# Optimization experiments

Measured on AMD Instinct MI355X. Metric: run time of the kernel, lower is better.

## Reference

```python
import jax, jax.numpy as jnp
import numpy as np

N = 50000
D = 128
E = 625000
EPS = 1e-15
BALL_EPS = 1e-5


def _logmap0(x, c):
    # Poincare ball log map at origin: artanh(sqrt(c)||x||) * x / (sqrt(c)||x||)
    sqrt_c = jnp.sqrt(c)
    xn = jnp.clip(jnp.linalg.norm(x, axis=-1, keepdims=True), EPS)
    arg = jnp.clip(sqrt_c * xn, -1.0 + BALL_EPS, 1.0 - BALL_EPS)
    return jnp.arctanh(arg) * x / (sqrt_c * xn)


def _expmap0(u, c):
    # Poincare ball exp map at origin: tanh(sqrt(c)||u||) * u / (sqrt(c)||u||)
    sqrt_c = jnp.sqrt(c)
    un = jnp.clip(jnp.linalg.norm(u, axis=-1, keepdims=True), EPS)
    return jnp.tanh(sqrt_c * un) * u / (sqrt_c * un)


def setup_inputs() -> dict:
    key = jax.random.key(0)
    ks = jax.random.split(key, 10)
    scale = 0.01  # keep points well inside the Poincare ball
    node_embeddings = jax.random.normal(ks[0], (N, D), jnp.float32) * scale
    hist1 = jax.random.normal(ks[1], (N, D), jnp.float32) * scale
    hist2 = jax.random.normal(ks[2], (N, D), jnp.float32) * scale
    hist3 = jax.random.normal(ks[3], (N, D), jnp.float32) * scale
    lin_w = jax.random.normal(ks[4], (D, D), jnp.float32) * (1.0 / np.sqrt(D))
    lin_b = jnp.zeros((D,), jnp.float32)
    conv_w = jax.random.normal(ks[5], (D, D, 3), jnp.float32) * (1.0 / np.sqrt(3 * D))
    conv_b = jnp.zeros((D,), jnp.float32)
    curvature = jnp.array([-1.0], jnp.float32)
    edge_src = jax.random.randint(ks[6], (E,), 0, N, jnp.int32)
    edge_dst = jax.random.randint(ks[7], (E,), 0, N, jnp.int32)
    return {
        'node_embeddings': node_embeddings,
        'hist1': hist1, 'hist2': hist2, 'hist3': hist3,
        'lin_w': lin_w, 'lin_b': lin_b,
        'conv_w': conv_w, 'conv_b': conv_b,
        'curvature': curvature,
        'edge_src': edge_src, 'edge_dst': edge_dst,
    }


def reference(node_embeddings, hist1, hist2, hist3, lin_w, lin_b,
              conv_w, conv_b, curvature, edge_src, edge_dst):
    c = jnp.abs(curvature[0])

    # --- HyperbolicDiffusionGraphConv ---
    tangent = _logmap0(node_embeddings, c)                       # [N, D]
    transformed = tangent @ lin_w.T + lin_b                      # [N, D]
    msgs = transformed[edge_src]                                 # [E, D] gather
    summed = jax.ops.segment_sum(msgs, edge_dst, num_segments=N)  # [N, D] scatter
    deg = jax.ops.segment_sum(jnp.ones((E,), jnp.float32), edge_dst, num_segments=N)
    neigh = jnp.where(deg[:, None] > 0, summed / jnp.clip(deg[:, None], 1.0), 0.0)
    current_emb = _expmap0(neigh, c)                             # [N, D]

    # --- HyperbolicDilatedCausalConv (3-step history, kernel_size=3 -> length 1) ---
    tangent_cur = _logmap0(current_emb, c)
    th = jnp.stack([_logmap0(hist1, c), _logmap0(hist2, c), _logmap0(hist3, c)], axis=2)  # [N, D, 3]
    # Conv1d(D -> D, k=3) on length-3 input reduces to a single contraction.
    conv_out = jnp.einsum('nik,oik->no', th, conv_w) + conv_b    # [N, D]
    return _expmap0(conv_out + tangent_cur, c)
```

## Files before the change

kernel.cpp:

```cpp
#include <hip/hip_runtime.h>

#define N_NODES 50000
#define DIM 128
#define N_EDGES 625000
#define EBLK 2442
#define SLOTS 96
#define CSTRIDE 16

#define SC_BLOCKS 25000
#define PK_BLOCKS 256
#define ZR_BLOCKS 196
#define SETUP_BLOCKS (SC_BLOCKS + PK_BLOCKS + ZR_BLOCKS)

typedef float f32x4 __attribute__((ext_vector_type(4)));
typedef short s16x8 __attribute__((ext_vector_type(8)));

__device__ __forceinline__ unsigned short f2bf(float f) {
    unsigned u = __builtin_bit_cast(unsigned, f);
    unsigned r = (u + 0x7fffu + ((u >> 16) & 1u)) >> 16;
    return (unsigned short)r;
}
__device__ __forceinline__ float lo_bf(unsigned u) {
    return __builtin_bit_cast(float, u << 16);
}
__device__ __forceinline__ float hi_bf(unsigned u) {
    return __builtin_bit_cast(float, u & 0xffff0000u);
}

__device__ __forceinline__ void gload_lds16(const unsigned short* g, unsigned short* l) {
    __builtin_amdgcn_global_load_lds(
        (const __attribute__((address_space(1))) void*)g,
        (__attribute__((address_space(3))) void*)l, 16, 0, 0);
}

__device__ __forceinline__ float logmap_scale(float ss, float sc) {
    float xn = fmaxf(sqrtf(ss), 1e-15f);
    float arg = fminf(sc * xn, 1.0f - 1e-5f);
    if (arg < 0.25f) {
        float z2 = arg * arg;
        return 1.0f + z2 * (0.33333333f + z2 * (0.2f + z2 * 0.14285715f));
    }
    float at = 0.5f * log1pf(2.0f * arg / (1.0f - arg));
    return at / (sc * xn);
}

__global__ __launch_bounds__(256) void k_setup(
    const float* __restrict__ node, const float* __restrict__ h1,
    const float* __restrict__ h2, const float* __restrict__ h3,
    const float* __restrict__ lin_w, const float* __restrict__ conv_w,
    const float* __restrict__ curv,
    unsigned short* __restrict__ node_t, unsigned short* __restrict__ A,
    unsigned short* __restrict__ Wt, int* __restrict__ cnt) {
    int b = blockIdx.x;
    int tid = threadIdx.x;
    if (b < SC_BLOCKS) {
        int row = b * 8 + (tid >> 5);
        int g = tid & 31;
        int a = row / N_NODES;
        int n = row - a * N_NODES;
        const float* src = (a == 0) ? node : (a == 1) ? h1 : (a == 2) ? h2 : h3;
        float4 x = ((const float4*)&src[n * DIM])[g];
        float ss = x.x * x.x + x.y * x.y + x.z * x.z + x.w * x.w;
        ss += __shfl_xor(ss, 1, 64);
        ss += __shfl_xor(ss, 2, 64);
        ss += __shfl_xor(ss, 4, 64);
        ss += __shfl_xor(ss, 8, 64);
        ss += __shfl_xor(ss, 16, 64);
        float c = fabsf(curv[0]);
        float s = logmap_scale(ss, sqrtf(c));
        unsigned short o0 = f2bf(x.x * s), o1 = f2bf(x.y * s);
        unsigned short o2 = f2bf(x.z * s), o3 = f2bf(x.w * s);
        uint2 ov;
        ov.x = (unsigned)o0 | ((unsigned)o1 << 16);
        ov.y = (unsigned)o2 | ((unsigned)o3 << 16);
        if (a == 0) {
            *(uint2*)&node_t[n * DIM + g * 4] = ov;
        } else {
            *(uint2*)&A[n * 512 + a * 128 + g * 4] = ov;
        }
    } else if (b < SC_BLOCKS + PK_BLOCKS) {
        int idx = (b - SC_BLOCKS) * 256 + tid;
        int o = idx >> 9;
        int k = idx & 511;
        float v;
        if (k < 128) {
            v = lin_w[o * 128 + k];
        } else {
            int kk = (k - 128) >> 7;
            int i = (k - 128) & 127;
            v = conv_w[o * 384 + i * 3 + kk];
        }
        Wt[idx] = f2bf(v);
    } else {
        int i = (b - SC_BLOCKS - PK_BLOCKS) * 256 + tid;
        if (i < N_NODES) cnt[i * CSTRIDE] = 0;
    }
}

__global__ void k_bucket(const int* __restrict__ esrc, const int* __restrict__ edst,
                         int* __restrict__ cnt, unsigned short* __restrict__ slots) {
    int e = blockIdx.x * 256 + threadIdx.x;
    if (e >= N_EDGES) return;
    int d = edst[e];
    int pos = __hip_atomic_fetch_add(&cnt[d * CSTRIDE], 1, __ATOMIC_RELAXED,
                                     __HIP_MEMORY_SCOPE_AGENT);
    if (pos < SLOTS) slots[d * SLOTS + pos] = (unsigned short)esrc[e];
}

__global__ __launch_bounds__(256) void k_gather(
    const unsigned short* __restrict__ slots, const int* __restrict__ cnt,
    const unsigned short* __restrict__ node_t, unsigned short* __restrict__ A) {
    int n = blockIdx.x * 8 + (threadIdx.x >> 5);
    int lane = threadIdx.x & 31;
    int ctrue = cnt[n * CSTRIDE];
    int c = ctrue < SLOTS ? ctrue : SLOTS;
    const unsigned short* row = &slots[n * SLOTS];
    float p0 = 0.f, p1 = 0.f, p2 = 0.f, p3 = 0.f;
    float q0 = 0.f, q1 = 0.f, q2 = 0.f, q3 = 0.f;
    for (int base = 0; base < c; base += 32) {
        int rem = c - base;
        int m = rem < 32 ? rem : 32;
        int my = (int)row[base + (lane < m ? lane : m - 1)];
        for (int i = 0; i < m; i += 8) {
            int i1 = i + 1 < m ? i + 1 : m - 1;
            int i2 = i + 2 < m ? i + 2 : m - 1;
            int i3 = i + 3 < m ? i + 3 : m - 1;
            int i4 = i + 4 < m ? i + 4 : m - 1;
            int i5 = i + 5 < m ? i + 5 : m - 1;
            int i6 = i + 6 < m ? i + 6 : m - 1;
            int i7 = i + 7 < m ? i + 7 : m - 1;
            int s0 = __shfl(my, i, 32),  s1 = __shfl(my, i1, 32);
            int s2 = __shfl(my, i2, 32), s3 = __shfl(my, i3, 32);
            int s4 = __shfl(my, i4, 32), s5 = __shfl(my, i5, 32);
            int s6 = __shfl(my, i6, 32), s7 = __shfl(my, i7, 32);
            uint2 u0 = *(const uint2*)&node_t[s0 * DIM + lane * 4];
            uint2 u1 = *(const uint2*)&node_t[s1 * DIM + lane * 4];
            uint2 u2 = *(const uint2*)&node_t[s2 * DIM + lane * 4];
            uint2 u3 = *(const uint2*)&node_t[s3 * DIM + lane * 4];
            uint2 u4 = *(const uint2*)&node_t[s4 * DIM + lane * 4];
            uint2 u5 = *(const uint2*)&node_t[s5 * DIM + lane * 4];
            uint2 u6 = *(const uint2*)&node_t[s6 * DIM + lane * 4];
            uint2 u7 = *(const uint2*)&node_t[s7 * DIM + lane * 4];
            p0 += lo_bf(u0.x); p1 += hi_bf(u0.x); p2 += lo_bf(u0.y); p3 += hi_bf(u0.y);
            if (i + 1 < m) { q0 += lo_bf(u1.x); q1 += hi_bf(u1.x); q2 += lo_bf(u1.y); q3 += hi_bf(u1.y); }
            if (i + 2 < m) { p0 += lo_bf(u2.x); p1 += hi_bf(u2.x); p2 += lo_bf(u2.y); p3 += hi_bf(u2.y); }
            if (i + 3 < m) { q0 += lo_bf(u3.x); q1 += hi_bf(u3.x); q2 += lo_bf(u3.y); q3 += hi_bf(u3.y); }
            if (i + 4 < m) { p0 += lo_bf(u4.x); p1 += hi_bf(u4.x); p2 += lo_bf(u4.y); p3 += hi_bf(u4.y); }
            if (i + 5 < m) { q0 += lo_bf(u5.x); q1 += hi_bf(u5.x); q2 += lo_bf(u5.y); q3 += hi_bf(u5.y); }
            if (i + 6 < m) { p0 += lo_bf(u6.x); p1 += hi_bf(u6.x); p2 += lo_bf(u6.y); p3 += hi_bf(u6.y); }
            if (i + 7 < m) { q0 += lo_bf(u7.x); q1 += hi_bf(u7.x); q2 += lo_bf(u7.y); q3 += hi_bf(u7.y); }
        }
    }
    float t0 = p0 + q0, t1 = p1 + q1, t2 = p2 + q2, t3 = p3 + q3;
    float inv = (ctrue > 0) ? 1.0f / (float)ctrue : 0.0f;
    unsigned short o0 = f2bf(t0 * inv), o1 = f2bf(t1 * inv);
    unsigned short o2 = f2bf(t2 * inv), o3 = f2bf(t3 * inv);
    uint2 ov;
    ov.x = (unsigned)o0 | ((unsigned)o1 << 16);
    ov.y = (unsigned)o2 | ((unsigned)o3 << 16);
    *(uint2*)&A[n * 512 + lane * 4] = ov;
}

#define RB 128
#define BK 64
__global__ __launch_bounds__(256) void k_gemm(
    const unsigned short* __restrict__ A, const int* __restrict__ deg,
    const unsigned short* __restrict__ Wt,
    const float* __restrict__ lin_b, const float* __restrict__ conv_b,
    const float* __restrict__ curv, float* __restrict__ out) {
    __shared__ __align__(16) unsigned short As[2][RB * BK];
    __shared__ __align__(16) unsigned short Bs[2][128 * BK];
    int tid = threadIdx.x;
    int n0 = blockIdx.x * RB;
    int w = tid >> 6;
    int lane = tid & 63;
    int ml = lane & 15;
    int q = lane >> 4;
    int lr = lane >> 3;
    int lj = lane & 7;

    f32x4 acc[2][8];
    #pragma unroll
    for (int rt = 0; rt < 2; ++rt)
        #pragma unroll
        for (int i = 0; i < 8; ++i) acc[rt][i] = (f32x4){0.f, 0.f, 0.f, 0.f};

    #pragma unroll
    for (int t = 0; t < 4; ++t) {
        int m = t * 4 + w;
        int r = m * 8 + lr;
        int jg = lj ^ (r & 7);
        gload_lds16(A + (n0 + r) * 512 + jg * 8, &As[0][m * 512]);
    }
    #pragma unroll
    for (int t = 0; t < 4; ++t) {
        int m = t * 4 + w;
        int r = m * 8 + lr;
        int jg = lj ^ (r & 7);
        gload_lds16(Wt + r * 512 + jg * 8, &Bs[0][m * 512]);
    }

    #pragma unroll
    for (int kk = 0; kk < 8; ++kk) {
        int cur = kk & 1;
        __syncthreads();
        if (kk < 7) {
            int nb = cur ^ 1;
            #pragma unroll
            for (int t = 0; t < 4; ++t) {
                int m = t * 4 + w;
                int r = m * 8 + lr;
                int jg = lj ^ (r & 7);
                gload_lds16(A + (n0 + r) * 512 + (kk + 1) * 64 + jg * 8, &As[nb][m * 512]);
            }
            #pragma unroll
            for (int t = 0; t < 4; ++t) {
                int m = t * 4 + w;
                int r = m * 8 + lr;
                int jg = lj ^ (r & 7);
                gload_lds16(Wt + r * 512 + (kk + 1) * 64 + jg * 8, &Bs[nb][m * 512]);
            }
        }
        __builtin_amdgcn_s_setprio(1);
        #pragma unroll
        for (int ks = 0; ks < 2; ++ks) {
            int ca = ((ks * 4 + q) ^ (ml & 7)) * 8;
            s16x8 a0 = *(const s16x8*)&As[cur][(w * 32 + ml) * BK + ca];
            s16x8 a1 = *(const s16x8*)&As[cur][(w * 32 + 16 + ml) * BK + ca];
            #pragma unroll
            for (int ct = 0; ct < 8; ++ct) {
                s16x8 bb = *(const s16x8*)&Bs[cur][(ct * 16 + ml) * BK + ca];
                acc[0][ct] = __builtin_amdgcn_mfma_f32_16x16x32_bf16(a0, bb, acc[0][ct], 0, 0, 0);
                acc[1][ct] = __builtin_amdgcn_mfma_f32_16x16x32_bf16(a1, bb, acc[1][ct], 0, 0, 0);
            }
        }
        __builtin_amdgcn_s_setprio(0);
    }

    float c = fabsf(curv[0]);
    float sc = sqrtf(c);
    float cb[8], lb[8];
    #pragma unroll
    for (int ct = 0; ct < 8; ++ct) {
        cb[ct] = conv_b[ct * 16 + ml];
        lb[ct] = lin_b[ct * 16 + ml];
    }
    #pragma unroll
    for (int rt = 0; rt < 2; ++rt) {
        #pragma unroll
        for (int r = 0; r < 4; ++r) {
            int n = n0 + w * 32 + rt * 16 + q * 4 + r;
            bool valid = (n < N_NODES);
            float dgf = 0.f;
            if (valid) dgf = (deg[n * CSTRIDE] > 0) ? 1.0f : 0.0f;
            float y[8];
            float ssq = 0.f;
            #pragma unroll
            for (int ct = 0; ct < 8; ++ct) {
                float v = acc[rt][ct][r] + cb[ct] + dgf * lb[ct];
                y[ct] = v;
                ssq += v * v;
            }
            ssq += __shfl_xor(ssq, 1, 64);
            ssq += __shfl_xor(ssq, 2, 64);
            ssq += __shfl_xor(ssq, 4, 64);
            ssq += __shfl_xor(ssq, 8, 64);
            float un = fmaxf(sqrtf(ssq), 1e-15f);
            float z = sc * un;
            float os;
            if (z < 0.25f) {
                float z2 = z * z;
                os = 1.0f + z2 * (-0.33333333f + z2 * (0.13333333f - z2 * 0.053968254f));
            } else {
                os = tanhf(z) / z;
            }
            if (valid) {
                #pragma unroll
                for (int ct = 0; ct < 8; ++ct)
                    out[n * DIM + ct * 16 + ml] = y[ct] * os;
            }
        }
    }
}

extern "C" void kernel_launch(void* const* d_in, const int* in_sizes, int n_in,
                              void* d_out, int out_size, void* d_ws, size_t ws_size,
                              hipStream_t stream) {
    (void)in_sizes; (void)n_in; (void)out_size; (void)ws_size;
    const float* node   = (const float*)d_in[0];
    const float* h1     = (const float*)d_in[1];
    const float* h2     = (const float*)d_in[2];
    const float* h3     = (const float*)d_in[3];
    const float* lin_w  = (const float*)d_in[4];
    const float* lin_b  = (const float*)d_in[5];
    const float* conv_w = (const float*)d_in[6];
    const float* conv_b = (const float*)d_in[7];
    const float* curv   = (const float*)d_in[8];
    const int* esrc = (const int*)d_in[9];
    const int* edst = (const int*)d_in[10];
    float* out = (float*)d_out;

    char* ws = (char*)d_ws;
    unsigned short* A = (unsigned short*)ws;
    unsigned short* node_t = (unsigned short*)(ws + 51200000);
    unsigned short* Wt = (unsigned short*)(ws + 64000000);
    int* cnt = (int*)(ws + 64131072);
    unsigned short* slots = (unsigned short*)(ws + 67331072);

    hipLaunchKernelGGL(k_setup, dim3(SETUP_BLOCKS), dim3(256), 0, stream,
                       node, h1, h2, h3, lin_w, conv_w, curv,
                       node_t, A, Wt, cnt);
    hipLaunchKernelGGL(k_bucket, dim3(EBLK), dim3(256), 0, stream,
                       esrc, edst, cnt, slots);
    hipLaunchKernelGGL(k_gather, dim3(6250), dim3(256), 0, stream,
                       slots, cnt, node_t, A);
    hipLaunchKernelGGL(k_gemm, dim3((N_NODES + RB - 1) / RB), dim3(256), 0, stream,
                       A, cnt, Wt, lin_b, conv_b, curv, out);
}
```

Measured before the change: 228.1 us.

## Fuse edge bucketing into setup kernel with interleaved blocks, memset counters

Merges the edge-bucketing kernel into the setup kernel by interleaving one bucketing block after every ten setup blocks, so the atomic-heavy bucketing overlaps with the bandwidth-bound logmap/bf16 conversion work. Counter zeroing moves to a hipMemsetAsync issued before the fused kernel, which is what makes the merge correct. The manual bf16 packing is also replaced with the packed conversion intrinsic. This removes one kernel launch and its serialization point, at the cost of an extra memset call and mixed block types in one grid.

```diff
diff --git a/kernel.cpp b/kernel.cpp
--- a/kernel.cpp
+++ b/kernel.cpp
@@ -1,4 +1,5 @@
 #include <hip/hip_runtime.h>
+#include <hip/hip_bf16.h>
 
 #define N_NODES 50000
 #define DIM 128
@@ -9,8 +10,9 @@
 
 #define SC_BLOCKS 25000
 #define PK_BLOCKS 256
-#define ZR_BLOCKS 196
-#define SETUP_BLOCKS (SC_BLOCKS + PK_BLOCKS + ZR_BLOCKS)
+#define OT_BLOCKS (SC_BLOCKS + PK_BLOCKS)
+#define IL_SPAN (EBLK * 11)
+#define SB_BLOCKS (OT_BLOCKS + EBLK)
 
 typedef float f32x4 __attribute__((ext_vector_type(4)));
 typedef short s16x8 __attribute__((ext_vector_type(8)));
@@ -19,6 +21,11 @@
     unsigned u = __builtin_bit_cast(unsigned, f);
     unsigned r = (u + 0x7fffu + ((u >> 16) & 1u)) >> 16;
     return (unsigned short)r;
+}
+__device__ __forceinline__ unsigned cvtpk_bf16(float lo, float hi) {
+    union { __hip_bfloat162 h; unsigned u; } cv;
+    cv.h = __float22bfloat162_rn(make_float2(lo, hi));
+    return cv.u;
 }
 __device__ __forceinline__ float lo_bf(unsigned u) {
     return __builtin_bit_cast(float, u << 16);
@@ -44,17 +51,38 @@
     return at / (sc * xn);
 }
 
-__global__ __launch_bounds__(256) void k_setup(
+__global__ __launch_bounds__(256) void k_sb(
     const float* __restrict__ node, const float* __restrict__ h1,
     const float* __restrict__ h2, const float* __restrict__ h3,
     const float* __restrict__ lin_w, const float* __restrict__ conv_w,
     const float* __restrict__ curv,
+    const int* __restrict__ esrc, const int* __restrict__ edst,
     unsigned short* __restrict__ node_t, unsigned short* __restrict__ A,
-    unsigned short* __restrict__ Wt, int* __restrict__ cnt) {
+    unsigned short* __restrict__ Wt, int* __restrict__ cnt,
+    unsigned short* __restrict__ slots) {
     int b = blockIdx.x;
     int tid = threadIdx.x;
-    if (b < SC_BLOCKS) {
-        int row = b * 8 + (tid >> 5);
+    int ot;
+    if (b < IL_SPAN) {
+        int q = b / 11;
+        int r = b - q * 11;
+        if (r == 5) {
+            int e = q * 256 + tid;
+            if (e < N_EDGES) {
+                int d = edst[e];
+                int pos = __hip_atomic_fetch_add(&cnt[d * CSTRIDE], 1,
+                                                 __ATOMIC_RELAXED,
+                                                 __HIP_MEMORY_SCOPE_AGENT);
+                if (pos < SLOTS) slots[d * SLOTS + pos] = (unsigned short)esrc[e];
+            }
+            return;
+        }
+        ot = q * 10 + (r < 5 ? r : r - 1);
+    } else {
+        ot = 24420 + (b - IL_SPAN);
+    }
+    if (ot < SC_BLOCKS) {
+        int row = ot * 8 + (tid >> 5);
         int g = tid & 31;
         int a = row / N_NODES;
         int n = row - a * N_NODES;
@@ -68,18 +96,16 @@
         ss += __shfl_xor(ss, 16, 64);
         float c = fabsf(curv[0]);
         float s = logmap_scale(ss, sqrtf(c));
-        unsigned short o0 = f2bf(x.x * s), o1 = f2bf(x.y * s);
-        unsigned short o2 = f2bf(x.z * s), o3 = f2bf(x.w * s);
         uint2 ov;
-        ov.x = (unsigned)o0 | ((unsigned)o1 << 16);
-        ov.y = (unsigned)o2 | ((unsigned)o3 << 16);
+        ov.x = cvtpk_bf16(x.x * s, x.y * s);
+        ov.y = cvtpk_bf16(x.z * s, x.w * s);
         if (a == 0) {
             *(uint2*)&node_t[n * DIM + g * 4] = ov;
         } else {
             *(uint2*)&A[n * 512 + a * 128 + g * 4] = ov;
         }
-    } else if (b < SC_BLOCKS + PK_BLOCKS) {
-        int idx = (b - SC_BLOCKS) * 256 + tid;
+    } else {
+        int idx = (ot - SC_BLOCKS) * 256 + tid;
         int o = idx >> 9;
         int k = idx & 511;
         float v;
@@ -91,20 +117,7 @@
             v = conv_w[o * 384 + i * 3 + kk];
         }
         Wt[idx] = f2bf(v);
-    } else {
-        int i = (b - SC_BLOCKS - PK_BLOCKS) * 256 + tid;
-        if (i < N_NODES) cnt[i * CSTRIDE] = 0;
-    }
-}
-
-__global__ void k_bucket(const int* __restrict__ esrc, const int* __restrict__ edst,
-                         int* __restrict__ cnt, unsigned short* __restrict__ slots) {
-    int e = blockIdx.x * 256 + threadIdx.x;
-    if (e >= N_EDGES) return;
-    int d = edst[e];
-    int pos = __hip_atomic_fetch_add(&cnt[d * CSTRIDE], 1, __ATOMIC_RELAXED,
-                                     __HIP_MEMORY_SCOPE_AGENT);
-    if (pos < SLOTS) slots[d * SLOTS + pos] = (unsigned short)esrc[e];
+    }
 }
 
 __global__ __launch_bounds__(256) void k_gather(
@@ -153,11 +166,9 @@
     }
     float t0 = p0 + q0, t1 = p1 + q1, t2 = p2 + q2, t3 = p3 + q3;
     float inv = (ctrue > 0) ? 1.0f / (float)ctrue : 0.0f;
-    unsigned short o0 = f2bf(t0 * inv), o1 = f2bf(t1 * inv);
-    unsigned short o2 = f2bf(t2 * inv), o3 = f2bf(t3 * inv);
     uint2 ov;
-    ov.x = (unsigned)o0 | ((unsigned)o1 << 16);
-    ov.y = (unsigned)o2 | ((unsigned)o3 << 16);
+    ov.x = cvtpk_bf16(t0 * inv, t1 * inv);
+    ov.y = cvtpk_bf16(t2 * inv, t3 * inv);
     *(uint2*)&A[n * 512 + lane * 4] = ov;
 }
 
@@ -307,11 +318,10 @@
     int* cnt = (int*)(ws + 64131072);
     unsigned short* slots = (unsigned short*)(ws + 67331072);
 
-    hipLaunchKernelGGL(k_setup, dim3(SETUP_BLOCKS), dim3(256), 0, stream,
-                       node, h1, h2, h3, lin_w, conv_w, curv,
-                       node_t, A, Wt, cnt);
-    hipLaunchKernelGGL(k_bucket, dim3(EBLK), dim3(256), 0, stream,
-                       esrc, edst, cnt, slots);
+    (void)hipMemsetAsync(cnt, 0, N_NODES * CSTRIDE * sizeof(int), stream);
+    hipLaunchKernelGGL(k_sb, dim3(SB_BLOCKS), dim3(256), 0, stream,
+                       node, h1, h2, h3, lin_w, conv_w, curv, esrc, edst,
+                       node_t, A, Wt, cnt, slots);
     hipLaunchKernelGGL(k_gather, dim3(6250), dim3(256), 0, stream,
                        slots, cnt, node_t, A);
     hipLaunchKernelGGL(k_gemm, dim3((N_NODES + RB - 1) / RB), dim3(256), 0, stream,
```

Result: faster. 206.5 us (-9.5%).
